# Performance work log

Hardware: AMD Instinct MI355X
Metric: run time of the kernel (lower is better)

Reference implementation:

```python
import jax, jax.numpy as jnp
import numpy as np

B, S, E = 4, 4096, 1024
H = 16
D = E // H            # per-head dim (k_dim == v_dim == 64)
N_SAMPLE = 1024       # tokens kept per (batch, head)


def setup_inputs() -> dict:
    key = jax.random.key(0)
    ks = jax.random.split(key, 7)
    lim = float(np.sqrt(6.0 / (E + E)))  # xavier_uniform for square weight
    x = jax.random.normal(ks[0], (B, S, E), dtype=jnp.float32)
    Wq = jax.random.uniform(ks[1], (E, E), jnp.float32, -lim, lim)
    Wk = jax.random.uniform(ks[2], (E, E), jnp.float32, -lim, lim)
    Wv = jax.random.uniform(ks[3], (E, E), jnp.float32, -lim, lim)
    bq = jnp.zeros((E,), jnp.float32)
    bk = jnp.zeros((E,), jnp.float32)
    bv = jnp.zeros((E,), jnp.float32)
    return {"x": x, "Wq": Wq, "bq": bq, "Wk": Wk, "bk": bk, "Wv": Wv, "bv": bv}


def reference(x, Wq, bq, Wk, bk, Wv, bv):
    Bs, Sl, Ed = x.shape
    # projections -> [B, H, S, D]
    q = (x @ Wq.T + bq).reshape(Bs, Sl, H, D).transpose(0, 2, 1, 3)
    k = (x @ Wk.T + bk).reshape(Bs, Sl, H, D).transpose(0, 2, 1, 3)
    v = (x @ Wv.T + bv).reshape(Bs, Sl, H, D).transpose(0, 2, 1, 3)

    # cosFormer feature map: relu + cos/sin positional reweighting
    pos = jnp.arange(Sl, dtype=x.dtype)
    theta = (jnp.pi / 2.0) * pos / Sl            # [S]
    cos_w = jnp.cos(theta)[None, None, :, None]  # [1,1,S,1]
    sin_w = jnp.sin(theta)[None, None, :, None]
    qn = jax.nn.relu(q)
    kn = jax.nn.relu(k)
    q_cos, q_sin = qn * cos_w, qn * sin_w
    k_cos, k_sin = kn * cos_w, kn * sin_w

    # token sampler: top-N_SAMPLE tokens by (q*k).sum(-1) per (b,h)
    scores = jnp.sum(q * k, axis=-1)             # [B,H,S]
    _, idx = jax.lax.top_k(scores, N_SAMPLE)     # [B,H,n]

    # global K^T V reductions: [B,H,D,D]
    kv_cos = jnp.einsum("bhsd,bhse->bhde", k_cos, v)
    kv_sin = jnp.einsum("bhsd,bhse->bhde", k_sin, v)

    # gather sampled queries: [B,H,n,D]
    qs_cos = jnp.take_along_axis(q_cos, idx[..., None], axis=2)
    qs_sin = jnp.take_along_axis(q_sin, idx[..., None], axis=2)

    sampled = (jnp.einsum("bhnd,bhde->bhne", qs_cos, kv_cos)
               + jnp.einsum("bhnd,bhde->bhne", qs_sin, kv_sin))  # [B,H,n,D]

    # scatter-add back into zeros at sampled positions
    bi = jnp.arange(Bs)[:, None, None]
    hi = jnp.arange(H)[None, :, None]
    values = jnp.zeros((Bs, H, Sl, D), sampled.dtype).at[bi, hi, idx].add(sampled)

    out = values.transpose(0, 2, 1, 3).reshape(Bs, Sl, H * D)
    return out  # o_proj is Identity (v_dim*num_heads == embed_dim); dropout=0
```

## Files before the change

### kernel.cpp

```cpp
#include <hip/hip_runtime.h>
#include <hip/hip_bf16.h>

#define B_ 4
#define S_ 4096
#define E_ 1024
#define H_ 16
#define D_ 64
#define NS_ 1024
#define M_ (B_*S_)
#define K_ E_
#define DELTA 0.12f
#define BANDCAP 96

typedef __attribute__((ext_vector_type(8))) short bf16x8;
typedef __attribute__((ext_vector_type(4))) float floatx4;
typedef __attribute__((ext_vector_type(2))) float f32x2;

#define THSTEP 0.00038349519697141023f

__device__ inline float bf16_to_f(unsigned short u) {
    return __uint_as_float(((unsigned)u) << 16);
}
__device__ inline unsigned short f_to_bf16(float f) {
    unsigned u = __float_as_uint(f);
    unsigned r = (u + 0x7FFFu + ((u >> 16) & 1u)) >> 16;
    return (unsigned short)r;
}

__device__ inline void gl_lds16(const void* g, void* l) {
    __builtin_amdgcn_global_load_lds(
        (const __attribute__((address_space(1))) void*)g,
        (__attribute__((address_space(3))) void*)l, 16, 0, 0);
}

__global__ __launch_bounds__(256) void prep_kernel(
    const float* __restrict__ x,
    const float* __restrict__ Wq, const float* __restrict__ Wk,
    const float* __restrict__ Wv,
    ushort* __restrict__ xh,
    ushort* __restrict__ Wqh, ushort* __restrict__ Wql,
    ushort* __restrict__ Wkh, ushort* __restrict__ Wkl,
    ushort* __restrict__ Wvh,
    uint4* __restrict__ outz)
{
    int t = blockIdx.x * 256 + threadIdx.x;
    uint4 z = make_uint4(0u, 0u, 0u, 0u);
#pragma unroll
    for (int c = 0; c < 4; ++c)
        outz[c * 1048576 + t] = z;
#pragma unroll
    for (int c = 0; c < 4; ++c) {
        int i = c * 1048576 + t;
        float4 v = ((const float4*)x)[i];
        ushort4 hh;
        hh.x = f_to_bf16(v.x); hh.y = f_to_bf16(v.y);
        hh.z = f_to_bf16(v.z); hh.w = f_to_bf16(v.w);
        ((ushort4*)xh)[i] = hh;
    }
    if (t < 262144) {
        int i = t;
        float4 q = ((const float4*)Wq)[i];
        float4 k = ((const float4*)Wk)[i];
        float4 v = ((const float4*)Wv)[i];
        ushort4 h, l;
        h.x=f_to_bf16(q.x); l.x=f_to_bf16(q.x-bf16_to_f(h.x));
        h.y=f_to_bf16(q.y); l.y=f_to_bf16(q.y-bf16_to_f(h.y));
        h.z=f_to_bf16(q.z); l.z=f_to_bf16(q.z-bf16_to_f(h.z));
        h.w=f_to_bf16(q.w); l.w=f_to_bf16(q.w-bf16_to_f(h.w));
        ((ushort4*)Wqh)[i]=h; ((ushort4*)Wql)[i]=l;
        h.x=f_to_bf16(k.x); l.x=f_to_bf16(k.x-bf16_to_f(h.x));
        h.y=f_to_bf16(k.y); l.y=f_to_bf16(k.y-bf16_to_f(h.y));
        h.z=f_to_bf16(k.z); l.z=f_to_bf16(k.z-bf16_to_f(h.z));
        h.w=f_to_bf16(k.w); l.w=f_to_bf16(k.w-bf16_to_f(h.w));
        ((ushort4*)Wkh)[i]=h; ((ushort4*)Wkl)[i]=l;
        h.x=f_to_bf16(v.x); h.y=f_to_bf16(v.y);
        h.z=f_to_bf16(v.z); h.w=f_to_bf16(v.w);
        ((ushort4*)Wvh)[i]=h;
    }
}

__global__ __launch_bounds__(256) void qkv_gemm(
    const ushort* __restrict__ xh,
    const ushort* __restrict__ Wqh, const ushort* __restrict__ Wql,
    const ushort* __restrict__ Wkh, const ushort* __restrict__ Wkl,
    const ushort* __restrict__ Wvh,
    const float* __restrict__ bq, const float* __restrict__ bk,
    const float* __restrict__ bv,
    float* __restrict__ q32, float* __restrict__ k32, ushort* __restrict__ v16)
{
    __shared__ __align__(16) ushort As[128 * 64];
    __shared__ __align__(16) ushort Bsh[128 * 64];
    __shared__ __align__(16) ushort Bsl[128 * 64];

    const int w = blockIdx.z;
    const ushort* Bhp = (w == 0) ? Wqh : (w == 1) ? Wkh : Wvh;
    const ushort* Blp = (w == 0) ? Wql : Wkl;
    const float* bias = (w == 0) ? bq : (w == 1) ? bk : bv;
    const bool lo = (w < 2);

    const int m0 = blockIdx.x * 128;
    const int n0 = blockIdx.y * 128;
    const int t = threadIdx.x;
    const int wave = t >> 6, lane = t & 63;
    const int wm = (wave >> 1) * 64, wn = (wave & 1) * 64;
    const int m16 = lane & 15, quad = lane >> 4;

    floatx4 acc[4][4];
#pragma unroll
    for (int i = 0; i < 4; i++)
#pragma unroll
        for (int j = 0; j < 4; j++) acc[i][j] = (floatx4){0.f, 0.f, 0.f, 0.f};

    int aoff[4], boff[4], lbase[4];
#pragma unroll
    for (int i = 0; i < 4; i++) {
        int slot = i * 256 + t;
        int r = slot >> 3, c = slot & 7, g = c ^ (r & 7);
        aoff[i] = (m0 + r) * K_ + g * 8;
        boff[i] = (n0 + r) * K_ + g * 8;
        lbase[i] = (i * 256 + wave * 64) * 8;
    }

    for (int ks = 0; ks < 16; ++ks) {
        const int kcol = ks * 64;
#pragma unroll
        for (int i = 0; i < 4; i++) {
            gl_lds16(xh + aoff[i] + kcol, &As[lbase[i]]);
            gl_lds16(Bhp + boff[i] + kcol, &Bsh[lbase[i]]);
        }
        if (lo) {
#pragma unroll
            for (int i = 0; i < 4; i++)
                gl_lds16(Blp + boff[i] + kcol, &Bsl[lbase[i]]);
        }
        __syncthreads();

#pragma unroll
        for (int kk = 0; kk < 2; ++kk) {
            bf16x8 af[4], bfr[4];
            const int g = kk * 4 + quad;
#pragma unroll
            for (int mt = 0; mt < 4; ++mt) {
                int r = wm + mt * 16 + m16;
                af[mt] = *(const bf16x8*)&As[(r * 8 + (g ^ (r & 7))) * 8];
            }
#pragma unroll
            for (int nt = 0; nt < 4; ++nt) {
                int r2 = wn + nt * 16 + m16;
                bfr[nt] = *(const bf16x8*)&Bsh[(r2 * 8 + (g ^ (r2 & 7))) * 8];
            }
#pragma unroll
            for (int mt = 0; mt < 4; ++mt)
#pragma unroll
                for (int nt = 0; nt < 4; ++nt)
                    acc[mt][nt] = __builtin_amdgcn_mfma_f32_16x16x32_bf16(
                        af[mt], bfr[nt], acc[mt][nt], 0, 0, 0);
            if (lo) {
#pragma unroll
                for (int nt = 0; nt < 4; ++nt) {
                    int r2 = wn + nt * 16 + m16;
                    bfr[nt] = *(const bf16x8*)&Bsl[(r2 * 8 + (g ^ (r2 & 7))) * 8];
                }
#pragma unroll
                for (int mt = 0; mt < 4; ++mt)
#pragma unroll
                    for (int nt = 0; nt < 4; ++nt)
                        acc[mt][nt] = __builtin_amdgcn_mfma_f32_16x16x32_bf16(
                            af[mt], bfr[nt], acc[mt][nt], 0, 0, 0);
            }
        }
        __syncthreads();
    }

    float biasv[4];
#pragma unroll
    for (int nt = 0; nt < 4; nt++)
        biasv[nt] = bias[n0 + wn + nt * 16 + m16];

    if (w < 2) {
        float* dst = (w == 0) ? q32 : k32;
#pragma unroll
        for (int mt = 0; mt < 4; ++mt)
#pragma unroll
            for (int nt = 0; nt < 4; ++nt) {
                int colg = n0 + wn + nt * 16 + m16;
#pragma unroll
                for (int reg = 0; reg < 4; ++reg) {
                    int rowg = m0 + wm + mt * 16 + quad * 4 + reg;
                    dst[(size_t)rowg * E_ + colg] = acc[mt][nt][reg] + biasv[nt];
                }
            }
    } else {
#pragma unroll
        for (int mt = 0; mt < 4; ++mt)
#pragma unroll
            for (int nt = 0; nt < 4; ++nt) {
                int colg = n0 + wn + nt * 16 + m16;
#pragma unroll
                for (int reg = 0; reg < 4; ++reg) {
                    int rowg = m0 + wm + mt * 16 + quad * 4 + reg;
                    v16[(size_t)rowg * E_ + colg] = f_to_bf16(acc[mt][nt][reg] + biasv[nt]);
                }
            }
    }
}

__global__ __launch_bounds__(256) void scores_kernel(
    const float* __restrict__ q32, const float* __restrict__ k32,
    float* __restrict__ scores)
{
    int g = blockIdx.x * 16 + (threadIdx.x >> 4);
    int sub = threadIdx.x & 15;
    int s = g & (S_ - 1);
    int bh = g >> 12;
    int b = bh >> 4, h = bh & 15;
    size_t addr = (size_t)(b * S_ + s) * E_ + h * 64 + sub * 4;
    float4 qv = *(const float4*)(q32 + addr);
    float4 kv = *(const float4*)(k32 + addr);
    float p = qv.x * kv.x + qv.y * kv.y + qv.z * kv.z + qv.w * kv.w;
#pragma unroll
    for (int m = 8; m; m >>= 1) p += __shfl_xor(p, m, 64);
    if (sub == 0) scores[g] = p;
}

__global__ __launch_bounds__(256) void band_select_kernel(
    const float* __restrict__ scores, int* __restrict__ selidx,
    int* __restrict__ band, int* __restrict__ meta)
{
    __shared__ unsigned keys[4096];
    __shared__ unsigned hist[256];
    __shared__ unsigned wtot[4];
    __shared__ unsigned bcast[2];
    __shared__ int cnt_in, cnt_band;

    int bh = blockIdx.x;
    int t = threadIdx.x;
    int wave = t >> 6, lane = t & 63;
    const float* sc = scores + (size_t)bh * S_;

    for (int i = t; i < 4096; i += 256) {
        unsigned u = __float_as_uint(sc[i]);
        u = (u & 0x80000000u) ? ~u : (u | 0x80000000u);
        keys[i] = u;
    }
    if (t == 0) { cnt_in = 0; cnt_band = 0; }

    unsigned prefix = 0, want = NS_;
    for (int shift = 24; shift >= 0; shift -= 8) {
        hist[t] = 0;
        __syncthreads();
        unsigned pmask = (shift == 24) ? 0u : (0xFFFFFFFFu << (shift + 8));
        for (int i = t; i < 4096; i += 256) {
            unsigned ky = keys[i];
            if ((ky & pmask) == prefix) atomicAdd(&hist[(ky >> shift) & 255u], 1u);
        }
        __syncthreads();
        unsigned sv = hist[t];
#pragma unroll
        for (int off = 1; off < 64; off <<= 1) {
            unsigned o = __shfl_down(sv, off, 64);
            sv += (lane + off < 64) ? o : 0u;
        }
        if (lane == 0) wtot[wave] = sv;
        __syncthreads();
        unsigned cross = 0;
#pragma unroll
        for (int w2 = 0; w2 < 4; ++w2)
            cross += (w2 > wave) ? wtot[w2] : 0u;
        unsigned Sb = sv + cross;
        unsigned sv1 = __shfl_down(sv, 1, 64);
        unsigned Snx = (lane < 63) ? sv1 + cross : cross;
        if (Sb >= want && Snx < want) {
            bcast[0] = (unsigned)t;
            bcast[1] = want - Snx;
        }
        __syncthreads();
        prefix = prefix | (bcast[0] << shift);
        want = bcast[1];
        __syncthreads();
    }
    unsigned fb = (prefix & 0x80000000u) ? (prefix ^ 0x80000000u) : ~prefix;
    float Ta = __uint_as_float(fb);
    float Thi = Ta + DELTA, Tlo = Ta - DELTA;

    int* sel = selidx + (size_t)bh * NS_;
    int* bnd = band + (size_t)bh * BANDCAP;
    for (int i = t; i < 4096; i += 256) {
        float v = sc[i];
        if (v > Thi) {
            int p = atomicAdd(&cnt_in, 1);
            sel[p] = i;
        } else if (v >= Tlo) {
            int p = atomicAdd(&cnt_band, 1);
            if (p < BANDCAP) bnd[p] = i;
        }
    }
    __syncthreads();
    if (t == 0) {
        meta[bh * 2 + 0] = cnt_in;
        meta[bh * 2 + 1] = (cnt_band < BANDCAP) ? cnt_band : BANDCAP;
    }
}

__global__ __launch_bounds__(512) void band_exact_kernel(
    const float* __restrict__ x,
    const float* __restrict__ Wq, const float* __restrict__ Wk,
    const int* __restrict__ band, const int* __restrict__ meta,
    double* __restrict__ bscore)
{
    int j = blockIdx.x, bh = blockIdx.y;
    int NB = meta[bh * 2 + 1];
    if (j >= NB) return;
    int b = bh >> 4, h = bh & 15;
    int s = band[(size_t)bh * BANDCAP + j];
    int t = threadIdx.x;
    int wave = t >> 6, lane = t & 63;

    __shared__ float xs[1024];
    __shared__ double qkd[128];

    if (t < 256)
        *(float4*)&xs[t * 4] = *(const float4*)(x + (size_t)(b * S_ + s) * K_ + t * 4);
    __syncthreads();

    const float* Wbase = (wave < 4) ? Wq : Wk;
    int role = wave >> 2;
    int dbase = (wave & 3) * 16;
    const float4* xs4 = (const float4*)xs;

    for (int rr = 0; rr < 16; ++rr) {
        int d = dbase + rr;
        const float4* wrow4 = (const float4*)(Wbase + (size_t)(h * 64 + d) * K_);
        double a0 = 0.0, a1 = 0.0, a2 = 0.0, a3 = 0.0;
#pragma unroll
        for (int p = 0; p < 4; ++p) {
            float4 wv = wrow4[lane + 64 * p];
            float4 xv = xs4[lane + 64 * p];
            a0 += (double)xv.x * wv.x;
            a1 += (double)xv.y * wv.y;
            a2 += (double)xv.z * wv.z;
            a3 += (double)xv.w * wv.w;
        }
        double a = (a0 + a1) + (a2 + a3);
#pragma unroll
        for (int m = 32; m; m >>= 1) a += __shfl_xor(a, m, 64);
        if (lane == 0) qkd[role * 64 + d] = a;
    }
    __syncthreads();

    if (t < 64) {
        double p = qkd[t] * qkd[64 + t];
#pragma unroll
        for (int m = 32; m; m >>= 1) p += __shfl_xor(p, m, 64);
        if (t == 0) bscore[(size_t)bh * BANDCAP + j] = p;
    }
}

__global__ __launch_bounds__(128) void band_rank_kernel(
    const double* __restrict__ bscore, const int* __restrict__ band,
    const int* __restrict__ meta, int* __restrict__ selidx)
{
    __shared__ double sc[BANDCAP];
    __shared__ int bi[BANDCAP];
    int bh = blockIdx.x, t = threadIdx.x;
    int cnt_in = meta[bh * 2 + 0], NB = meta[bh * 2 + 1];
    int need = NS_ - cnt_in;
    if (t < NB) {
        sc[t] = bscore[(size_t)bh * BANDCAP + t];
        bi[t] = band[(size_t)bh * BANDCAP + t];
    }
    __syncthreads();
    if (t < NB) {
        double mine = sc[t]; int myi = bi[t]; int r = 0;
        for (int j2 = 0; j2 < NB; ++j2)
            r += (sc[j2] > mine) || (sc[j2] == mine && bi[j2] < myi);
        if (r < need) selidx[(size_t)bh * NS_ + cnt_in + r] = myi;
    }
}

__global__ __launch_bounds__(256) void kv_mfma_kernel(
    const float* __restrict__ k32, const ushort* __restrict__ v16,
    float* __restrict__ kvp)
{
    __shared__ __align__(16) ushort P[5 * 64 * 88];

    const int ch = blockIdx.x;
    const int bh = blockIdx.y;
    const int b = bh >> 4, h = bh & 15;
    const int t = threadIdx.x;
    const int wave = t >> 6, lane = t & 63;
    const int m16 = lane & 15, quad = lane >> 4;
    const int wm = (wave >> 1) * 32, wn = (wave & 1) * 32;
    const int d0 = wave * 16;

    const float*  kbase = k32 + (size_t)b * S_ * E_ + h * 64 + d0;
    const ushort* vbase = v16 + (size_t)b * S_ * E_ + h * 64 + d0;

    floatx4 acc[2][2][2];
#pragma unroll
    for (int p = 0; p < 2; p++)
#pragma unroll
        for (int i = 0; i < 2; i++)
#pragma unroll
            for (int j = 0; j < 2; j++) acc[p][i][j] = (floatx4){0.f,0.f,0.f,0.f};

    float  ka[16];
    ushort va[16];
    int sg = ch * 256 + lane;
    {
        const float*  kr = kbase + (size_t)sg * E_;
        const ushort* vr = vbase + (size_t)sg * E_;
#pragma unroll
        for (int j = 0; j < 4; ++j) *(float4*)&ka[j * 4] = ((const float4*)kr)[j];
        *(uint4*)&va[0] = *(const uint4*)vr;
        *(uint4*)&va[8] = *(const uint4*)(vr + 8);
    }

    for (int grp = 0; grp < 4; ++grp) {
        float th = (float)sg * THSTEP;
        float cw = __cosf(th), sw = __sinf(th);
        int s_loc = lane;

        __syncthreads();
#pragma unroll
        for (int j = 0; j < 16; ++j) {
            float kr_ = fmaxf(ka[j], 0.f);
            float pc = kr_ * cw, ps = kr_ * sw;
            ushort chh = f_to_bf16(pc);
            ushort cll = f_to_bf16(pc - bf16_to_f(chh));
            ushort shh = f_to_bf16(ps);
            ushort sll = f_to_bf16(ps - bf16_to_f(shh));
            int r = (d0 + j) * 88 + s_loc;
            P[0 * 5632 + r] = chh;
            P[1 * 5632 + r] = cll;
            P[2 * 5632 + r] = shh;
            P[3 * 5632 + r] = sll;
            P[4 * 5632 + r] = va[j];
        }
        __syncthreads();

        if (grp < 3) {
            sg += 64;
            const float*  kr = kbase + (size_t)sg * E_;
            const ushort* vr = vbase + (size_t)sg * E_;
#pragma unroll
            for (int j = 0; j < 4; ++j) *(float4*)&ka[j * 4] = ((const float4*)kr)[j];
            *(uint4*)&va[0] = *(const uint4*)vr;
            *(uint4*)&va[8] = *(const uint4*)(vr + 8);
        }

#pragma unroll
        for (int kk = 0; kk < 2; ++kk) {
            const int so = kk * 32 + quad * 8;
            bf16x8 ach[2], acl[2], ash[2], asl[2], bv[2];
#pragma unroll
            for (int mt = 0; mt < 2; ++mt) {
                int r = (wm + mt * 16 + m16) * 88 + so;
                ach[mt] = *(const bf16x8*)&P[0 * 5632 + r];
                acl[mt] = *(const bf16x8*)&P[1 * 5632 + r];
                ash[mt] = *(const bf16x8*)&P[2 * 5632 + r];
                asl[mt] = *(const bf16x8*)&P[3 * 5632 + r];
            }
#pragma unroll
            for (int nt = 0; nt < 2; ++nt) {
                int r = (wn + nt * 16 + m16) * 88 + so;
                bv[nt] = *(const bf16x8*)&P[4 * 5632 + r];
            }
#pragma unroll
            for (int mt = 0; mt < 2; ++mt)
#pragma unroll
                for (int nt = 0; nt < 2; ++nt) {
                    acc[0][mt][nt] = __builtin_amdgcn_mfma_f32_16x16x32_bf16(
                        ach[mt], bv[nt], acc[0][mt][nt], 0, 0, 0);
                    acc[0][mt][nt] = __builtin_amdgcn_mfma_f32_16x16x32_bf16(
                        acl[mt], bv[nt], acc[0][mt][nt], 0, 0, 0);
                    acc[1][mt][nt] = __builtin_amdgcn_mfma_f32_16x16x32_bf16(
                        ash[mt], bv[nt], acc[1][mt][nt], 0, 0, 0);
                    acc[1][mt][nt] = __builtin_amdgcn_mfma_f32_16x16x32_bf16(
                        asl[mt], bv[nt], acc[1][mt][nt], 0, 0, 0);
                }
        }
    }

    float* base = kvp + ((size_t)(bh * 16 + ch) * 2) * 4096;
#pragma unroll
    for (int p = 0; p < 2; ++p)
#pragma unroll
        for (int mt = 0; mt < 2; ++mt)
#pragma unroll
            for (int nt = 0; nt < 2; ++nt)
#pragma unroll
                for (int reg = 0; reg < 4; ++reg) {
                    int row = wm + mt * 16 + quad * 4 + reg;
                    int col = wn + nt * 16 + m16;
                    base[p * 4096 + row * 64 + col] = acc[p][mt][nt][reg];
                }
}

__global__ __launch_bounds__(256) void kv_reduce_kernel(
    const float* __restrict__ kvp, float* __restrict__ kv)
{
    int i = blockIdx.x * 256 + threadIdx.x;
    if (i >= 64 * 2 * 4096) return;
    int bh = i >> 13;
    int rem = i & 8191;
    const float* p = kvp + (size_t)bh * 16 * 8192 + rem;
    float a = 0.f;
#pragma unroll
    for (int c = 0; c < 16; c++) a += p[c * 8192];
    kv[i] = a;
}

__global__ __launch_bounds__(256) void sampled_kernel(
    const float* __restrict__ q32, const int* __restrict__ selidx,
    const float* __restrict__ kv, float* __restrict__ out)
{
    __shared__ __align__(16) float kvc[4096];
    __shared__ __align__(16) float kvs[4096];
    __shared__ __align__(16) float qs[64 * 68];
    __shared__ int sidx[64];
    int bh = blockIdx.y;
    int b = bh >> 4, h = bh & 15;
    int t = threadIdx.x;

    const float4* kvsrc4 = (const float4*)(kv + (size_t)bh * 8192);
    float4* kvc4 = (float4*)kvc;
    float4* kvs4 = (float4*)kvs;
#pragma unroll
    for (int i = 0; i < 4; ++i) {
        kvc4[i * 256 + t] = kvsrc4[i * 256 + t];
        kvs4[i * 256 + t] = kvsrc4[1024 + i * 256 + t];
    }
    if (t < 64) sidx[t] = selidx[(size_t)bh * NS_ + blockIdx.x * 64 + t];
    __syncthreads();

#pragma unroll
    for (int c = 0; c < 4; ++c) {
        int i = c * 256 + t;
        int row = i >> 4, qp = i & 15;
        int sr = sidx[row];
        *(float4*)&qs[row * 68 + qp * 4] =
            *(const float4*)(q32 + (size_t)(b * S_ + sr) * E_ + h * 64 + qp * 4);
    }
    __syncthreads();

    int tok = t >> 2, eq = t & 3;
    int sr = sidx[tok];
    float th = (float)sr * THSTEP;
    float cw = __cosf(th), sw = __sinf(th);

    f32x2 acc2[8];
#pragma unroll
    for (int e = 0; e < 8; e++) acc2[e] = (f32x2){0.f, 0.f};

    const float4* kvcb = (const float4*)&kvc[eq * 16];
    const float4* kvsb = (const float4*)&kvs[eq * 16];
    for (int d = 0; d < 64; ++d) {
        float qd = fmaxf(qs[tok * 68 + d], 0.f);
        f32x2 a2 = { qd * cw, qd * cw };
        f32x2 b2 = { qd * sw, qd * sw };
#pragma unroll
        for (int c = 0; c < 4; ++c) {
            float4 c4 = kvcb[d * 16 + c];
            float4 s4 = kvsb[d * 16 + c];
            f32x2 c01 = { c4.x, c4.y }, c23 = { c4.z, c4.w };
            f32x2 s01 = { s4.x, s4.y }, s23 = { s4.z, s4.w };
            acc2[c * 2 + 0] += a2 * c01 + b2 * s01;
            acc2[c * 2 + 1] += a2 * c23 + b2 * s23;
        }
    }

    float* dst = out + (size_t)(b * S_ + sr) * E_ + h * 64 + eq * 16;
#pragma unroll
    for (int c = 0; c < 4; ++c) {
        float4 o = { acc2[c * 2 + 0][0], acc2[c * 2 + 0][1],
                     acc2[c * 2 + 1][0], acc2[c * 2 + 1][1] };
        *(float4*)(dst + c * 4) = o;
    }
}

extern "C" void kernel_launch(void* const* d_in, const int* in_sizes, int n_in,
                              void* d_out, int out_size, void* d_ws, size_t ws_size,
                              hipStream_t stream)
{
    const float* x  = (const float*)d_in[0];
    const float* Wq = (const float*)d_in[1];
    const float* bq = (const float*)d_in[2];
    const float* Wk = (const float*)d_in[3];
    const float* bk = (const float*)d_in[4];
    const float* Wv = (const float*)d_in[5];
    const float* bv = (const float*)d_in[6];

    char* ws = (char*)d_ws;
    ushort* xh     = (ushort*)(ws);
    float*  kvp    = (float*)(ws);
    float*  q32    = (float*)(ws + 33554432);
    float*  k32    = (float*)(ws + 100663296);
    ushort* v16    = (ushort*)(ws + 167772160);
    ushort* Wqh    = (ushort*)(ws + 201326592);
    ushort* Wql    = (ushort*)(ws + 203423744);
    ushort* Wkh    = (ushort*)(ws + 205520896);
    ushort* Wkl    = (ushort*)(ws + 207618048);
    ushort* Wvh    = (ushort*)(ws + 209715200);
    float*  scores = (float*)(ws + 211812352);
    int*    selidx = (int*)(ws + 212860928);
    int*    band   = (int*)(ws + 213123072);
    double* bscore = (double*)(ws + 213147648);
    int*    meta   = (int*)(ws + 213196800);
    float*  kv     = (float*)(ws + 213197312);
    float*  out    = (float*)d_out;

    hipLaunchKernelGGL(prep_kernel, dim3(4096), dim3(256), 0, stream,
                       x, Wq, Wk, Wv, xh, Wqh, Wql, Wkh, Wkl, Wvh, (uint4*)out);
    hipLaunchKernelGGL(qkv_gemm, dim3(128, 8, 3), dim3(256), 0, stream,
                       xh, Wqh, Wql, Wkh, Wkl, Wvh, bq, bk, bv, q32, k32, v16);
    hipLaunchKernelGGL(scores_kernel, dim3((B_ * H_ * S_) / 16), dim3(256), 0, stream,
                       q32, k32, scores);
    hipLaunchKernelGGL(band_select_kernel, dim3(B_ * H_), dim3(256), 0, stream,
                       scores, selidx, band, meta);
    hipLaunchKernelGGL(band_exact_kernel, dim3(BANDCAP, B_ * H_), dim3(512), 0, stream,
                       x, Wq, Wk, band, meta, bscore);
    hipLaunchKernelGGL(band_rank_kernel, dim3(B_ * H_), dim3(128), 0, stream,
                       bscore, band, meta, selidx);
    hipLaunchKernelGGL(kv_mfma_kernel, dim3(16, 64), dim3(256), 0, stream,
                       k32, v16, kvp);
    hipLaunchKernelGGL(kv_reduce_kernel, dim3(2048), dim3(256), 0, stream,
                       kvp, kv);
    hipLaunchKernelGGL(sampled_kernel, dim3(NS_ / 64, B_ * H_), dim3(256), 0, stream,
                       q32, selidx, kv, out);
}
```

Measured before the change: 501.6 us.

## Double-buffer QKV GEMM LDS tiles and merge independent kernels into combined launches

The QKV GEMM now uses a 32-wide K tile held in two LDS buffers, with the next tile prefetched while MFMAs run on the current one. This takes the load latency off the critical path at the cost of twice as many k-steps and barriers. Separately, the scores kernel is merged into the K^T V MFMA kernel, and the kv partial-sum reduction is merged with top-k band selection. Each pair is dispatched by block index in one launch, which cuts launch count and lets independent work run concurrently.

Measured after the change: 513.4 us. +2.3%, slower.

```diff
diff --git a/kernel.cpp b/kernel.cpp
--- a/kernel.cpp
+++ b/kernel.cpp
@@ -88,9 +88,9 @@
     const float* __restrict__ bv,
     float* __restrict__ q32, float* __restrict__ k32, ushort* __restrict__ v16)
 {
-    __shared__ __align__(16) ushort As[128 * 64];
-    __shared__ __align__(16) ushort Bsh[128 * 64];
-    __shared__ __align__(16) ushort Bsl[128 * 64];
+    __shared__ __align__(16) ushort As[2][128 * 32];
+    __shared__ __align__(16) ushort Bsh[2][128 * 32];
+    __shared__ __align__(16) ushort Bsl[2][128 * 32];
 
     const int w = blockIdx.z;
     const ushort* Bhp = (w == 0) ? Wqh : (w == 1) ? Wkh : Wvh;
@@ -111,63 +111,65 @@
 #pragma unroll
         for (int j = 0; j < 4; j++) acc[i][j] = (floatx4){0.f, 0.f, 0.f, 0.f};
 
-    int aoff[4], boff[4], lbase[4];
-#pragma unroll
-    for (int i = 0; i < 4; i++) {
+    int aoff[2], boff[2], lbase[2];
+#pragma unroll
+    for (int i = 0; i < 2; i++) {
         int slot = i * 256 + t;
-        int r = slot >> 3, c = slot & 7, g = c ^ (r & 7);
+        int r = slot >> 2, c = slot & 3, g = c ^ ((r >> 1) & 3);
         aoff[i] = (m0 + r) * K_ + g * 8;
         boff[i] = (n0 + r) * K_ + g * 8;
         lbase[i] = (i * 256 + wave * 64) * 8;
     }
 
-    for (int ks = 0; ks < 16; ++ks) {
-        const int kcol = ks * 64;
-#pragma unroll
-        for (int i = 0; i < 4; i++) {
-            gl_lds16(xh + aoff[i] + kcol, &As[lbase[i]]);
-            gl_lds16(Bhp + boff[i] + kcol, &Bsh[lbase[i]]);
-        }
+    int afo[4], bfo[4];
+#pragma unroll
+    for (int mt = 0; mt < 4; ++mt) {
+        int r = wm + mt * 16 + m16;
+        afo[mt] = (r * 4 + (quad ^ ((r >> 1) & 3))) * 8;
+        int r2 = wn + mt * 16 + m16;
+        bfo[mt] = (r2 * 4 + (quad ^ ((r2 >> 1) & 3))) * 8;
+    }
+
+#pragma unroll
+    for (int i = 0; i < 2; i++) {
+        gl_lds16(xh + aoff[i], &As[0][lbase[i]]);
+        gl_lds16(Bhp + boff[i], &Bsh[0][lbase[i]]);
+        if (lo) gl_lds16(Blp + boff[i], &Bsl[0][lbase[i]]);
+    }
+    __syncthreads();
+
+    for (int ks = 0; ks < 32; ++ks) {
+        const int cur = ks & 1;
+        if (ks < 31) {
+            const int kcol = (ks + 1) * 32;
+#pragma unroll
+            for (int i = 0; i < 2; i++) {
+                gl_lds16(xh + aoff[i] + kcol, &As[cur ^ 1][lbase[i]]);
+                gl_lds16(Bhp + boff[i] + kcol, &Bsh[cur ^ 1][lbase[i]]);
+                if (lo) gl_lds16(Blp + boff[i] + kcol, &Bsl[cur ^ 1][lbase[i]]);
+            }
+        }
+
+        bf16x8 af[4], bfr[4];
+#pragma unroll
+        for (int mt = 0; mt < 4; ++mt) af[mt] = *(const bf16x8*)&As[cur][afo[mt]];
+#pragma unroll
+        for (int nt = 0; nt < 4; ++nt) bfr[nt] = *(const bf16x8*)&Bsh[cur][bfo[nt]];
+#pragma unroll
+        for (int mt = 0; mt < 4; ++mt)
+#pragma unroll
+            for (int nt = 0; nt < 4; ++nt)
+                acc[mt][nt] = __builtin_amdgcn_mfma_f32_16x16x32_bf16(
+                    af[mt], bfr[nt], acc[mt][nt], 0, 0, 0);
         if (lo) {
 #pragma unroll
-            for (int i = 0; i < 4; i++)
-                gl_lds16(Blp + boff[i] + kcol, &Bsl[lbase[i]]);
-        }
-        __syncthreads();
-
-#pragma unroll
-        for (int kk = 0; kk < 2; ++kk) {
-            bf16x8 af[4], bfr[4];
-            const int g = kk * 4 + quad;
-#pragma unroll
-            for (int mt = 0; mt < 4; ++mt) {
-                int r = wm + mt * 16 + m16;
-                af[mt] = *(const bf16x8*)&As[(r * 8 + (g ^ (r & 7))) * 8];
-            }
-#pragma unroll
-            for (int nt = 0; nt < 4; ++nt) {
-                int r2 = wn + nt * 16 + m16;
-                bfr[nt] = *(const bf16x8*)&Bsh[(r2 * 8 + (g ^ (r2 & 7))) * 8];
-            }
+            for (int nt = 0; nt < 4; ++nt) bfr[nt] = *(const bf16x8*)&Bsl[cur][bfo[nt]];
 #pragma unroll
             for (int mt = 0; mt < 4; ++mt)
 #pragma unroll
                 for (int nt = 0; nt < 4; ++nt)
                     acc[mt][nt] = __builtin_amdgcn_mfma_f32_16x16x32_bf16(
                         af[mt], bfr[nt], acc[mt][nt], 0, 0, 0);
-            if (lo) {
-#pragma unroll
-                for (int nt = 0; nt < 4; ++nt) {
-                    int r2 = wn + nt * 16 + m16;
-                    bfr[nt] = *(const bf16x8*)&Bsl[(r2 * 8 + (g ^ (r2 & 7))) * 8];
-                }
-#pragma unroll
-                for (int mt = 0; mt < 4; ++mt)
-#pragma unroll
-                    for (int nt = 0; nt < 4; ++nt)
-                        acc[mt][nt] = __builtin_amdgcn_mfma_f32_16x16x32_bf16(
-                            af[mt], bfr[nt], acc[mt][nt], 0, 0, 0);
-            }
         }
         __syncthreads();
     }
@@ -205,189 +207,33 @@
     }
 }
 
-__global__ __launch_bounds__(256) void scores_kernel(
+__global__ __launch_bounds__(256) void scores_kv_kernel(
     const float* __restrict__ q32, const float* __restrict__ k32,
-    float* __restrict__ scores)
-{
-    int g = blockIdx.x * 16 + (threadIdx.x >> 4);
-    int sub = threadIdx.x & 15;
-    int s = g & (S_ - 1);
-    int bh = g >> 12;
-    int b = bh >> 4, h = bh & 15;
-    size_t addr = (size_t)(b * S_ + s) * E_ + h * 64 + sub * 4;
-    float4 qv = *(const float4*)(q32 + addr);
-    float4 kv = *(const float4*)(k32 + addr);
-    float p = qv.x * kv.x + qv.y * kv.y + qv.z * kv.z + qv.w * kv.w;
-#pragma unroll
-    for (int m = 8; m; m >>= 1) p += __shfl_xor(p, m, 64);
-    if (sub == 0) scores[g] = p;
-}
-
-__global__ __launch_bounds__(256) void band_select_kernel(
-    const float* __restrict__ scores, int* __restrict__ selidx,
-    int* __restrict__ band, int* __restrict__ meta)
-{
-    __shared__ unsigned keys[4096];
-    __shared__ unsigned hist[256];
-    __shared__ unsigned wtot[4];
-    __shared__ unsigned bcast[2];
-    __shared__ int cnt_in, cnt_band;
-
-    int bh = blockIdx.x;
-    int t = threadIdx.x;
-    int wave = t >> 6, lane = t & 63;
-    const float* sc = scores + (size_t)bh * S_;
-
-    for (int i = t; i < 4096; i += 256) {
-        unsigned u = __float_as_uint(sc[i]);
-        u = (u & 0x80000000u) ? ~u : (u | 0x80000000u);
-        keys[i] = u;
-    }
-    if (t == 0) { cnt_in = 0; cnt_band = 0; }
-
-    unsigned prefix = 0, want = NS_;
-    for (int shift = 24; shift >= 0; shift -= 8) {
-        hist[t] = 0;
-        __syncthreads();
-        unsigned pmask = (shift == 24) ? 0u : (0xFFFFFFFFu << (shift + 8));
-        for (int i = t; i < 4096; i += 256) {
-            unsigned ky = keys[i];
-            if ((ky & pmask) == prefix) atomicAdd(&hist[(ky >> shift) & 255u], 1u);
-        }
-        __syncthreads();
-        unsigned sv = hist[t];
-#pragma unroll
-        for (int off = 1; off < 64; off <<= 1) {
-            unsigned o = __shfl_down(sv, off, 64);
-            sv += (lane + off < 64) ? o : 0u;
-        }
-        if (lane == 0) wtot[wave] = sv;
-        __syncthreads();
-        unsigned cross = 0;
-#pragma unroll
-        for (int w2 = 0; w2 < 4; ++w2)
-            cross += (w2 > wave) ? wtot[w2] : 0u;
-        unsigned Sb = sv + cross;
-        unsigned sv1 = __shfl_down(sv, 1, 64);
-        unsigned Snx = (lane < 63) ? sv1 + cross : cross;
-        if (Sb >= want && Snx < want) {
-            bcast[0] = (unsigned)t;
-            bcast[1] = want - Snx;
-        }
-        __syncthreads();
-        prefix = prefix | (bcast[0] << shift);
-        want = bcast[1];
-        __syncthreads();
-    }
-    unsigned fb = (prefix & 0x80000000u) ? (prefix ^ 0x80000000u) : ~prefix;
-    float Ta = __uint_as_float(fb);
-    float Thi = Ta + DELTA, Tlo = Ta - DELTA;
-
-    int* sel = selidx + (size_t)bh * NS_;
-    int* bnd = band + (size_t)bh * BANDCAP;
-    for (int i = t; i < 4096; i += 256) {
-        float v = sc[i];
-        if (v > Thi) {
-            int p = atomicAdd(&cnt_in, 1);
-            sel[p] = i;
-        } else if (v >= Tlo) {
-            int p = atomicAdd(&cnt_band, 1);
-            if (p < BANDCAP) bnd[p] = i;
-        }
-    }
-    __syncthreads();
-    if (t == 0) {
-        meta[bh * 2 + 0] = cnt_in;
-        meta[bh * 2 + 1] = (cnt_band < BANDCAP) ? cnt_band : BANDCAP;
-    }
-}
-
-__global__ __launch_bounds__(512) void band_exact_kernel(
-    const float* __restrict__ x,
-    const float* __restrict__ Wq, const float* __restrict__ Wk,
-    const int* __restrict__ band, const int* __restrict__ meta,
-    double* __restrict__ bscore)
-{
-    int j = blockIdx.x, bh = blockIdx.y;
-    int NB = meta[bh * 2 + 1];
-    if (j >= NB) return;
-    int b = bh >> 4, h = bh & 15;
-    int s = band[(size_t)bh * BANDCAP + j];
-    int t = threadIdx.x;
-    int wave = t >> 6, lane = t & 63;
-
-    __shared__ float xs[1024];
-    __shared__ double qkd[128];
-
-    if (t < 256)
-        *(float4*)&xs[t * 4] = *(const float4*)(x + (size_t)(b * S_ + s) * K_ + t * 4);
-    __syncthreads();
-
-    const float* Wbase = (wave < 4) ? Wq : Wk;
-    int role = wave >> 2;
-    int dbase = (wave & 3) * 16;
-    const float4* xs4 = (const float4*)xs;
-
-    for (int rr = 0; rr < 16; ++rr) {
-        int d = dbase + rr;
-        const float4* wrow4 = (const float4*)(Wbase + (size_t)(h * 64 + d) * K_);
-        double a0 = 0.0, a1 = 0.0, a2 = 0.0, a3 = 0.0;
-#pragma unroll
-        for (int p = 0; p < 4; ++p) {
-            float4 wv = wrow4[lane + 64 * p];
-            float4 xv = xs4[lane + 64 * p];
-            a0 += (double)xv.x * wv.x;
-            a1 += (double)xv.y * wv.y;
-            a2 += (double)xv.z * wv.z;
-            a3 += (double)xv.w * wv.w;
-        }
-        double a = (a0 + a1) + (a2 + a3);
-#pragma unroll
-        for (int m = 32; m; m >>= 1) a += __shfl_xor(a, m, 64);
-        if (lane == 0) qkd[role * 64 + d] = a;
-    }
-    __syncthreads();
-
-    if (t < 64) {
-        double p = qkd[t] * qkd[64 + t];
-#pragma unroll
-        for (int m = 32; m; m >>= 1) p += __shfl_xor(p, m, 64);
-        if (t == 0) bscore[(size_t)bh * BANDCAP + j] = p;
-    }
-}
-
-__global__ __launch_bounds__(128) void band_rank_kernel(
-    const double* __restrict__ bscore, const int* __restrict__ band,
-    const int* __restrict__ meta, int* __restrict__ selidx)
-{
-    __shared__ double sc[BANDCAP];
-    __shared__ int bi[BANDCAP];
-    int bh = blockIdx.x, t = threadIdx.x;
-    int cnt_in = meta[bh * 2 + 0], NB = meta[bh * 2 + 1];
-    int need = NS_ - cnt_in;
-    if (t < NB) {
-        sc[t] = bscore[(size_t)bh * BANDCAP + t];
-        bi[t] = band[(size_t)bh * BANDCAP + t];
-    }
-    __syncthreads();
-    if (t < NB) {
-        double mine = sc[t]; int myi = bi[t]; int r = 0;
-        for (int j2 = 0; j2 < NB; ++j2)
-            r += (sc[j2] > mine) || (sc[j2] == mine && bi[j2] < myi);
-        if (r < need) selidx[(size_t)bh * NS_ + cnt_in + r] = myi;
-    }
-}
-
-__global__ __launch_bounds__(256) void kv_mfma_kernel(
-    const float* __restrict__ k32, const ushort* __restrict__ v16,
-    float* __restrict__ kvp)
+    const ushort* __restrict__ v16,
+    float* __restrict__ scores, float* __restrict__ kvp)
 {
     __shared__ __align__(16) ushort P[5 * 64 * 88];
-
-    const int ch = blockIdx.x;
-    const int bh = blockIdx.y;
+    const int t = threadIdx.x;
+
+    if (blockIdx.x >= 1024) {
+        int g = (blockIdx.x - 1024) * 16 + (t >> 4);
+        int sub = t & 15;
+        int s = g & (S_ - 1);
+        int bh = g >> 12;
+        int b = bh >> 4, h = bh & 15;
+        size_t addr = (size_t)(b * S_ + s) * E_ + h * 64 + sub * 4;
+        float4 qv = *(const float4*)(q32 + addr);
+        float4 kv = *(const float4*)(k32 + addr);
+        float p = qv.x * kv.x + qv.y * kv.y + qv.z * kv.z + qv.w * kv.w;
+#pragma unroll
+        for (int m = 8; m; m >>= 1) p += __shfl_xor(p, m, 64);
+        if (sub == 0) scores[g] = p;
+        return;
+    }
+
+    const int ch = blockIdx.x & 15;
+    const int bh = blockIdx.x >> 4;
     const int b = bh >> 4, h = bh & 15;
-    const int t = threadIdx.x;
     const int wave = t >> 6, lane = t & 63;
     const int m16 = lane & 15, quad = lane >> 4;
     const int wm = (wave >> 1) * 32, wn = (wave & 1) * 32;
@@ -497,18 +343,173 @@
                 }
 }
 
-__global__ __launch_bounds__(256) void kv_reduce_kernel(
-    const float* __restrict__ kvp, float* __restrict__ kv)
-{
-    int i = blockIdx.x * 256 + threadIdx.x;
-    if (i >= 64 * 2 * 4096) return;
-    int bh = i >> 13;
-    int rem = i & 8191;
-    const float* p = kvp + (size_t)bh * 16 * 8192 + rem;
-    float a = 0.f;
-#pragma unroll
-    for (int c = 0; c < 16; c++) a += p[c * 8192];
-    kv[i] = a;
+__global__ __launch_bounds__(256) void select_reduce_kernel(
+    const float* __restrict__ kvp, float* __restrict__ kv,
+    const float* __restrict__ scores, int* __restrict__ selidx,
+    int* __restrict__ band, int* __restrict__ meta)
+{
+    __shared__ unsigned keys[4096];
+    __shared__ unsigned hist[256];
+    __shared__ unsigned wtot[4];
+    __shared__ unsigned bcast[2];
+    __shared__ int cnt_in, cnt_band;
+
+    int t = threadIdx.x;
+
+    if (blockIdx.x < 2048) {
+        int i = blockIdx.x * 256 + t;
+        int bh = i >> 13;
+        int rem = i & 8191;
+        const float* p = kvp + (size_t)bh * 16 * 8192 + rem;
+        float a = 0.f;
+#pragma unroll
+        for (int c = 0; c < 16; c++) a += p[c * 8192];
+        kv[i] = a;
+        return;
+    }
+
+    int bh = blockIdx.x - 2048;
+    int wave = t >> 6, lane = t & 63;
+    const float* sc = scores + (size_t)bh * S_;
+
+    for (int i = t; i < 4096; i += 256) {
+        unsigned u = __float_as_uint(sc[i]);
+        u = (u & 0x80000000u) ? ~u : (u | 0x80000000u);
+        keys[i] = u;
+    }
+    if (t == 0) { cnt_in = 0; cnt_band = 0; }
+
+    unsigned prefix = 0, want = NS_;
+    for (int shift = 24; shift >= 0; shift -= 8) {
+        hist[t] = 0;
+        __syncthreads();
+        unsigned pmask = (shift == 24) ? 0u : (0xFFFFFFFFu << (shift + 8));
+        for (int i = t; i < 4096; i += 256) {
+            unsigned ky = keys[i];
+            if ((ky & pmask) == prefix) atomicAdd(&hist[(ky >> shift) & 255u], 1u);
+        }
+        __syncthreads();
+        unsigned sv = hist[t];
+#pragma unroll
+        for (int off = 1; off < 64; off <<= 1) {
+            unsigned o = __shfl_down(sv, off, 64);
+            sv += (lane + off < 64) ? o : 0u;
+        }
+        if (lane == 0) wtot[wave] = sv;
+        __syncthreads();
+        unsigned cross = 0;
+#pragma unroll
+        for (int w2 = 0; w2 < 4; ++w2)
+            cross += (w2 > wave) ? wtot[w2] : 0u;
+        unsigned Sb = sv + cross;
+        unsigned sv1 = __shfl_down(sv, 1, 64);
+        unsigned Snx = (lane < 63) ? sv1 + cross : cross;
+        if (Sb >= want && Snx < want) {
+            bcast[0] = (unsigned)t;
+            bcast[1] = want - Snx;
+        }
+        __syncthreads();
+        prefix = prefix | (bcast[0] << shift);
+        want = bcast[1];
+        __syncthreads();
+    }
+    unsigned fb = (prefix & 0x80000000u) ? (prefix ^ 0x80000000u) : ~prefix;
+    float Ta = __uint_as_float(fb);
+    float Thi = Ta + DELTA, Tlo = Ta - DELTA;
+
+    int* sel = selidx + (size_t)bh * NS_;
+    int* bnd = band + (size_t)bh * BANDCAP;
+    for (int i = t; i < 4096; i += 256) {
+        float v = sc[i];
+        if (v > Thi) {
+            int p = atomicAdd(&cnt_in, 1);
+            sel[p] = i;
+        } else if (v >= Tlo) {
+            int p = atomicAdd(&cnt_band, 1);
+            if (p < BANDCAP) bnd[p] = i;
+        }
+    }
+    __syncthreads();
+    if (t == 0) {
+        meta[bh * 2 + 0] = cnt_in;
+        meta[bh * 2 + 1] = (cnt_band < BANDCAP) ? cnt_band : BANDCAP;
+    }
+}
+
+__global__ __launch_bounds__(512) void band_exact_kernel(
+    const float* __restrict__ x,
+    const float* __restrict__ Wq, const float* __restrict__ Wk,
+    const int* __restrict__ band, const int* __restrict__ meta,
+    double* __restrict__ bscore)
+{
+    int j = blockIdx.x, bh = blockIdx.y;
+    int NB = meta[bh * 2 + 1];
+    if (j >= NB) return;
+    int b = bh >> 4, h = bh & 15;
+    int s = band[(size_t)bh * BANDCAP + j];
+    int t = threadIdx.x;
+    int wave = t >> 6, lane = t & 63;
+
+    __shared__ float xs[1024];
+    __shared__ double qkd[128];
+
+    if (t < 256)
+        *(float4*)&xs[t * 4] = *(const float4*)(x + (size_t)(b * S_ + s) * K_ + t * 4);
+    __syncthreads();
+
+    const float* Wbase = (wave < 4) ? Wq : Wk;
+    int role = wave >> 2;
+    int dbase = (wave & 3) * 16;
+    const float4* xs4 = (const float4*)xs;
+
+    for (int rr = 0; rr < 16; ++rr) {
+        int d = dbase + rr;
+        const float4* wrow4 = (const float4*)(Wbase + (size_t)(h * 64 + d) * K_);
+        double a0 = 0.0, a1 = 0.0, a2 = 0.0, a3 = 0.0;
+#pragma unroll
+        for (int p = 0; p < 4; ++p) {
+            float4 wv = wrow4[lane + 64 * p];
+            float4 xv = xs4[lane + 64 * p];
+            a0 += (double)xv.x * wv.x;
+            a1 += (double)xv.y * wv.y;
+            a2 += (double)xv.z * wv.z;
+            a3 += (double)xv.w * wv.w;
+        }
+        double a = (a0 + a1) + (a2 + a3);
+#pragma unroll
+        for (int m = 32; m; m >>= 1) a += __shfl_xor(a, m, 64);
+        if (lane == 0) qkd[role * 64 + d] = a;
+    }
+    __syncthreads();
+
+    if (t < 64) {
+        double p = qkd[t] * qkd[64 + t];
+#pragma unroll
+        for (int m = 32; m; m >>= 1) p += __shfl_xor(p, m, 64);
+        if (t == 0) bscore[(size_t)bh * BANDCAP + j] = p;
+    }
+}
+
+__global__ __launch_bounds__(128) void band_rank_kernel(
+    const double* __restrict__ bscore, const int* __restrict__ band,
+    const int* __restrict__ meta, int* __restrict__ selidx)
+{
+    __shared__ double sc[BANDCAP];
+    __shared__ int bi[BANDCAP];
+    int bh = blockIdx.x, t = threadIdx.x;
+    int cnt_in = meta[bh * 2 + 0], NB = meta[bh * 2 + 1];
+    int need = NS_ - cnt_in;
+    if (t < NB) {
+        sc[t] = bscore[(size_t)bh * BANDCAP + t];
+        bi[t] = band[(size_t)bh * BANDCAP + t];
+    }
+    __syncthreads();
+    if (t < NB) {
+        double mine = sc[t]; int myi = bi[t]; int r = 0;
+        for (int j2 = 0; j2 < NB; ++j2)
+            r += (sc[j2] > mine) || (sc[j2] == mine && bi[j2] < myi);
+        if (r < need) selidx[(size_t)bh * NS_ + cnt_in + r] = myi;
+    }
 }
 
 __global__ __launch_bounds__(256) void sampled_kernel(
@@ -614,18 +615,14 @@
                        x, Wq, Wk, Wv, xh, Wqh, Wql, Wkh, Wkl, Wvh, (uint4*)out);
     hipLaunchKernelGGL(qkv_gemm, dim3(128, 8, 3), dim3(256), 0, stream,
                        xh, Wqh, Wql, Wkh, Wkl, Wvh, bq, bk, bv, q32, k32, v16);
-    hipLaunchKernelGGL(scores_kernel, dim3((B_ * H_ * S_) / 16), dim3(256), 0, stream,
-                       q32, k32, scores);
-    hipLaunchKernelGGL(band_select_kernel, dim3(B_ * H_), dim3(256), 0, stream,
-                       scores, selidx, band, meta);
+    hipLaunchKernelGGL(scores_kv_kernel, dim3(1024 + 16384), dim3(256), 0, stream,
+                       q32, k32, v16, scores, kvp);
+    hipLaunchKernelGGL(select_reduce_kernel, dim3(2048 + 64), dim3(256), 0, stream,
+                       kvp, kv, scores, selidx, band, meta);
     hipLaunchKernelGGL(band_exact_kernel, dim3(BANDCAP, B_ * H_), dim3(512), 0, stream,
                        x, Wq, Wk, band, meta, bscore);
     hipLaunchKernelGGL(band_rank_kernel, dim3(B_ * H_), dim3(128), 0, stream,
                        bscore, band, meta, selidx);
-    hipLaunchKernelGGL(kv_mfma_kernel, dim3(16, 64), dim3(256), 0, stream,
-                       k32, v16, kvp);
-    hipLaunchKernelGGL(kv_reduce_kernel, dim3(2048), dim3(256), 0, stream,
-                       kvp, kv);
     hipLaunchKernelGGL(sampled_kernel, dim3(NS_ / 64, B_ * H_), dim3(256), 0, stream,
                        q32, selidx, kv, out);
 }
```
